# Kernel tuning notes

Measured on AMD Instinct MI355X. Metric: run time of the kernel, lower is better.

Reference implementation:

```python
import jax, jax.numpy as jnp
import numpy as np

E, D, I, TOPK, N = 8, 2048, 4096, 2, 4096


def setup_inputs() -> dict:
    key = jax.random.key(0)
    k_x, k_w, k_i, k_g, k_u, k_d = jax.random.split(key, 6)
    x = jax.random.normal(k_x, (N, D), dtype=jnp.float32)
    expert_weights = jax.random.uniform(k_w, (N, TOPK), dtype=jnp.float32)
    expert_indices = jax.random.randint(k_i, (N, TOPK), 0, E).astype(jnp.int32)
    s_in = np.float32(1.0 / np.sqrt(D))
    s_mid = np.float32(1.0 / np.sqrt(I))
    # SwitchLinear weights: [num_experts, out_features, in_features]
    wg = jax.random.normal(k_g, (E, I, D), dtype=jnp.float32) * s_in
    wu = jax.random.normal(k_u, (E, I, D), dtype=jnp.float32) * s_in
    wd = jax.random.normal(k_d, (E, D, I), dtype=jnp.float32) * s_mid
    return {"x": x, "expert_weights": expert_weights,
            "expert_indices": expert_indices, "top_k": TOPK,
            "wg": wg, "wu": wu, "wd": wd}


def reference(x, expert_weights, expert_indices, top_k, wg, wu, wd):
    # out[n] = sum_k expert_weights[n,k] * Wd[e] @ (silu(Wg[e] x[n]) * (Wu[e] x[n]))
    #          with e = expert_indices[n,k].
    # Grouped-by-expert form (identical math): accumulate each expert's
    # contribution over all tokens, weighted by its routing weight (0 if not routed).
    num_experts = wg.shape[0]
    out = jnp.zeros_like(x)
    for e in range(num_experts):
        # per-token routing weight for expert e (sums over top_k slots)
        w_e = jnp.sum(jnp.where(expert_indices == e, expert_weights, 0.0), axis=-1)  # [N]
        gate = x @ wg[e].T            # [N, I]
        up = x @ wu[e].T              # [N, I]
        h = jax.nn.silu(gate) * up    # SwiGLU, [N, I]
        out = out + w_e[:, None] * (h @ wd[e].T)  # [N, D]
    return out
```

## Files before the change

### kernel.cpp

```cpp
#include <hip/hip_runtime.h>
#include <hip/hip_bf16.h>
#include <math.h>

#define E_ 8
#define D_ 2048
#define I_ 4096
#define TOPK_ 2
#define N_ 4096
#define NPAIR (N_*TOPK_)
#define PADMAX 10240
#define MAXTB256 40
#define MAXTB128 72

typedef __attribute__((ext_vector_type(8))) short s8v;
typedef __attribute__((ext_vector_type(8))) unsigned short us8;
typedef __attribute__((ext_vector_type(4))) float f32x4;
typedef const __attribute__((address_space(1))) void* gvp;
typedef __attribute__((address_space(3))) void* lvp;

__device__ __forceinline__ unsigned short f2bf(float f) {
  union { float f; unsigned int u; } c; c.f = f;
  unsigned int u = c.u;
  u += 0x7fffu + ((u >> 16) & 1u);
  return (unsigned short)(u >> 16);
}

__global__ void route_kernel(const int* __restrict__ idx, const float* __restrict__ ew,
                             int pad,
                             int* cnt, int* offs, int* tb, int* ntb,
                             int* perm, float* wgt)
{
  __shared__ int scnt[E_], soff[E_ + 1], scur[E_];
  int t = threadIdx.x;
  if (t < E_) scnt[t] = 0;
  __syncthreads();
  for (int p = t; p < NPAIR; p += blockDim.x) atomicAdd(&scnt[idx[p]], 1);
  __syncthreads();
  if (t == 0) {
    int o = 0;
    for (int e = 0; e < E_; e++) {
      soff[e] = o; scur[e] = o;
      o += ((scnt[e] + pad - 1) / pad) * pad;
    }
    soff[E_] = o;
    int T = 0;
    for (int e = 0; e < E_; e++) {
      int nb = (scnt[e] + pad - 1) / pad;
      for (int rb = 0; rb < nb; rb++) tb[T++] = (e << 16) | rb;
    }
    *ntb = T;
    for (int e = 0; e < E_; e++) { cnt[e] = scnt[e]; offs[e] = soff[e]; }
    offs[E_] = o;
  }
  __syncthreads();
  for (int e = 0; e < E_; e++) {
    int start = soff[e] + scnt[e], end = soff[e + 1];
    for (int s = start + t; s < end; s += blockDim.x) { perm[s] = -1; wgt[s] = 0.f; }
  }
  __syncthreads();
  for (int p = t; p < NPAIR; p += blockDim.x) {
    int e = idx[p];
    int pos = atomicAdd(&scur[e], 1);
    perm[pos] = p / TOPK_;
    wgt[pos]  = ew[p];
  }
}

__global__ __launch_bounds__(256)
void cvt8_kernel(const float* __restrict__ src, unsigned short* __restrict__ dst)
{
  size_t i = ((size_t)blockIdx.x * 256 + threadIdx.x) * 8;
  float4 a = *(const float4*)(src + i);
  float4 b = *(const float4*)(src + i + 4);
  us8 o;
  o[0]=f2bf(a.x); o[1]=f2bf(a.y); o[2]=f2bf(a.z); o[3]=f2bf(a.w);
  o[4]=f2bf(b.x); o[5]=f2bf(b.y); o[6]=f2bf(b.z); o[7]=f2bf(b.w);
  *(us8*)(dst + i) = o;
}

__global__ __launch_bounds__(256)
void cvtw_kernel(const float* __restrict__ s0, const float* __restrict__ s1,
                 const float* __restrict__ s2,
                 unsigned short* __restrict__ d0, unsigned short* __restrict__ d1,
                 unsigned short* __restrict__ d2)
{
  int b = blockIdx.x;
  int which = b >> 15, bi = b & 32767;
  const float* s = which == 0 ? s0 : (which == 1 ? s1 : s2);
  unsigned short* d = which == 0 ? d0 : (which == 1 ? d1 : d2);
  size_t i = ((size_t)bi * 256 + threadIdx.x) * 8;
  float4 a = *(const float4*)(s + i);
  float4 bb = *(const float4*)(s + i + 4);
  us8 o;
  o[0]=f2bf(a.x); o[1]=f2bf(a.y); o[2]=f2bf(a.z); o[3]=f2bf(a.w);
  o[4]=f2bf(bb.x); o[5]=f2bf(bb.y); o[6]=f2bf(bb.z); o[7]=f2bf(bb.w);
  *(us8*)(d + i) = o;
}

#define A_SLAB(P,KH) (((P)*2+(KH))*8192)
#define B_SLAB(P,KH) (32768 + ((P)*2+(KH))*8192)

#define SB  __builtin_amdgcn_sched_barrier(0)
#define BARR __builtin_amdgcn_s_barrier()
#define VMW(N) asm volatile("s_waitcnt vmcnt(" #N ")" ::: "memory")
#define LGK asm volatile("s_waitcnt lgkmcnt(0)" ::: "memory")

#define LOAD_A(P,KH,MH) { \
  const unsigned short* ap_ = &smem[A_SLAB(P,KH) + aBase + (MH)*2048]; \
  af[0] = *(const s8v*)(ap_);      af[1] = *(const s8v*)(ap_+512); \
  af[2] = *(const s8v*)(ap_+1024); af[3] = *(const s8v*)(ap_+1536); }

#define LOAD_B(P,KH) { \
  const unsigned short* bp_ = &smem[B_SLAB(P,KH) + bBase]; \
  bf[0] = *(const s8v*)(bp_);      bf[1] = *(const s8v*)(bp_+512); \
  bf[2] = *(const s8v*)(bp_+1024); bf[3] = *(const s8v*)(bp_+1536); }

#define STAGE_A(T,KH,P) { \
  __builtin_amdgcn_global_load_lds((gvp)(aptr0 + (T)*64 + (KH)*32), (lvp)(&smem[A_SLAB(P,KH) + (w*2+0)*512]), 16, 0, 0); \
  __builtin_amdgcn_global_load_lds((gvp)(aptr1 + (T)*64 + (KH)*32), (lvp)(&smem[A_SLAB(P,KH) + (w*2+1)*512]), 16, 0, 0); }

#define STAGE_B(T,KH,P) { \
  __builtin_amdgcn_global_load_lds((gvp)(bptr0 + (T)*64 + (KH)*32), (lvp)(&smem[B_SLAB(P,KH) + (w*2+0)*512]), 16, 0, 0); \
  __builtin_amdgcn_global_load_lds((gvp)(bptr1 + (T)*64 + (KH)*32), (lvp)(&smem[B_SLAB(P,KH) + (w*2+1)*512]), 16, 0, 0); }

#define MFMA16(MH) { \
  _Pragma("unroll") for (int m_ = 0; m_ < 4; m_++) \
    _Pragma("unroll") for (int n_ = 0; n_ < 4; n_++) \
      acc[(MH)*4+m_][n_] = __builtin_amdgcn_mfma_f32_16x16x32_bf16(af[m_], bf[n_], acc[(MH)*4+m_][n_], 0, 0, 0); }

#define TILE_PHASES(T, P, Pn, NT_) { \
  if (T) { VMW(4); SB; } \
  LOAD_B(P, 0); LOAD_A(P, 0, 0); \
  if ((T) + 1 < (NT_)) { STAGE_A((T)+1, 1, Pn); } \
  SB; BARR; LGK; SB; \
  __builtin_amdgcn_s_setprio(1); MFMA16(0); __builtin_amdgcn_s_setprio(0); \
  SB; BARR; SB; \
  LOAD_A(P, 0, 1); \
  if ((T) + 1 < (NT_)) { STAGE_B((T)+1, 1, Pn); } \
  SB; BARR; LGK; SB; \
  __builtin_amdgcn_s_setprio(1); MFMA16(1); __builtin_amdgcn_s_setprio(0); \
  SB; BARR; SB; \
  if ((T) == (NT_) - 1) { VMW(0); SB; } else { VMW(4); SB; } \
  LOAD_B(P, 1); LOAD_A(P, 1, 0); \
  if ((T) + 2 < (NT_)) { STAGE_A((T)+2, 0, P); } \
  SB; BARR; LGK; SB; \
  __builtin_amdgcn_s_setprio(1); MFMA16(0); __builtin_amdgcn_s_setprio(0); \
  SB; BARR; SB; \
  LOAD_A(P, 1, 1); \
  if ((T) + 2 < (NT_)) { STAGE_B((T)+2, 0, P); } \
  SB; BARR; LGK; SB; \
  __builtin_amdgcn_s_setprio(1); MFMA16(1); __builtin_amdgcn_s_setprio(0); \
  SB; BARR; SB; }

#define K_LOOP(NT_) { \
  STAGE_A(0,0,0); STAGE_B(0,0,0); STAGE_A(0,1,0); STAGE_B(0,1,0); \
  STAGE_A(1,0,1); STAGE_B(1,0,1); \
  VMW(8); SB; BARR; SB; \
  _Pragma("unroll 1") \
  for (int tt = 0; tt < (NT_)/2; ++tt) { \
    int t0_ = 2*tt, t1_ = 2*tt+1; \
    TILE_PHASES(t0_, 0, 1, NT_); \
    TILE_PHASES(t1_, 1, 0, NT_); \
  } }

__global__ __launch_bounds__(512, 2)
void gu8_kernel(const unsigned short* __restrict__ xb,
                const unsigned short* __restrict__ wgb,
                const unsigned short* __restrict__ wub,
                const int* __restrict__ tb, const int* __restrict__ ntb,
                const int* __restrict__ offs, const int* __restrict__ perm,
                unsigned short* __restrict__ H)
{
  __shared__ unsigned short smem[65536];

  int nwg = gridDim.x * gridDim.y;
  int lid = blockIdx.y * gridDim.x + blockIdx.x;
  int cpx = nwg >> 3;
  int sid = (lid & 7) * cpx + (lid >> 3);
  int bx = sid % gridDim.x;
  int by = sid / gridDim.x;
  if (bx >= *ntb) return;
  int ent = tb[bx];
  int e = ent >> 16, rb = ent & 0xffff;
  int slotbase = offs[e] + rb * 256;
  int i0 = by * 128;

  int tid = threadIdx.x, lane = tid & 63, w = tid >> 6;
  int wr = w >> 2, wc = w & 3;

  int cS = (lane & 7) ^ (lane >> 3);
  int rrS = 2 * (lane >> 3) + (cS >> 2);
  int kcS = (cS & 3) * 8;
  int ar0 = (w * 2 + 0) * 16 + rrS;
  int tk0 = perm[slotbase + ar0];       if (tk0 < 0) tk0 = 0;
  int tk1 = perm[slotbase + ar0 + 16];  if (tk1 < 0) tk1 = 0;
  const unsigned short* aptr0 = xb + (size_t)tk0 * D_ + kcS;
  const unsigned short* aptr1 = xb + (size_t)tk1 * D_ + kcS;
  const unsigned short* bptr0 = wgb + ((size_t)e * I_ + i0 + w * 16 + rrS) * D_ + kcS;
  const unsigned short* bptr1 = wub + ((size_t)e * I_ + i0 + w * 16 + rrS) * D_ + kcS;

  int hl = (lane & 15) >> 1;
  int pA = (((lane & 1) * 4 + (lane >> 4)) ^ hl) * 8;
  int aBase = wr * 4096 + hl * 64 + pA;
  int bBase = wc * 2048 + hl * 64 + pA;

  s8v af[4], bf[4];
  f32x4 acc[8][4];
#pragma unroll
  for (int m = 0; m < 8; m++)
#pragma unroll
    for (int n = 0; n < 4; n++) acc[m][n] = f32x4{0.f,0.f,0.f,0.f};

  K_LOOP(32);

#pragma unroll
  for (int m = 0; m < 8; m++) {
#pragma unroll
    for (int r = 0; r < 4; r++) {
      int row = wr * 128 + m * 16 + (lane >> 4) * 4 + r;
      size_t hbase = (size_t)(slotbase + row) * I_ + i0 + (lane & 15);
#pragma unroll
      for (int pr = 0; pr < 2; pr++) {
        float g = acc[m][pr*2][r];
        float u = acc[m][pr*2+1][r];
        float h = (g / (1.0f + __expf(-g))) * u;
        H[hbase + (wc * 2 + pr) * 16] = f2bf(h);
      }
    }
  }
}

__global__ __launch_bounds__(512, 2)
void down8_kernel(const unsigned short* __restrict__ H,
                  const unsigned short* __restrict__ wdb,
                  const int* __restrict__ tb, const int* __restrict__ ntb,
                  const int* __restrict__ offs, const int* __restrict__ perm,
                  const float* __restrict__ wgt,
                  float* __restrict__ out)
{
  __shared__ unsigned short smem[65536];

  int nwg = gridDim.x * gridDim.y;
  int lid = blockIdx.y * gridDim.x + blockIdx.x;
  int cpx = nwg >> 3;
  int sid = (lid & 7) * cpx + (lid >> 3);
  int bx = sid % gridDim.x;
  int by = sid / gridDim.x;
  if (bx >= *ntb) return;
  int ent = tb[bx];
  int e = ent >> 16, rb = ent & 0xffff;
  int slotbase = offs[e] + rb * 256;
  int d0 = by * 256;

  int tid = threadIdx.x, lane = tid & 63, w = tid >> 6;
  int wr = w >> 2, wc = w & 3;

  int cS = (lane & 7) ^ (lane >> 3);
  int rrS = 2 * (lane >> 3) + (cS >> 2);
  int kcS = (cS & 3) * 8;
  int ar0 = (w * 2 + 0) * 16 + rrS;
  const unsigned short* aptr0 = H + (size_t)(slotbase + ar0) * I_ + kcS;
  const unsigned short* aptr1 = H + (size_t)(slotbase + ar0 + 16) * I_ + kcS;
  const unsigned short* bptr0 = wdb + ((size_t)e * D_ + d0 + (w*2+0)*16 + rrS) * I_ + kcS;
  const unsigned short* bptr1 = wdb + ((size_t)e * D_ + d0 + (w*2+1)*16 + rrS) * I_ + kcS;

  int hl = (lane & 15) >> 1;
  int pA = (((lane & 1) * 4 + (lane >> 4)) ^ hl) * 8;
  int aBase = wr * 4096 + hl * 64 + pA;
  int bBase = wc * 2048 + hl * 64 + pA;

  s8v af[4], bf[4];
  f32x4 acc[8][4];
#pragma unroll
  for (int m = 0; m < 8; m++)
#pragma unroll
    for (int n = 0; n < 4; n++) acc[m][n] = f32x4{0.f,0.f,0.f,0.f};

  K_LOOP(64);

#pragma unroll
  for (int m = 0; m < 8; m++) {
#pragma unroll
    for (int r = 0; r < 4; r++) {
      int row = wr * 128 + m * 16 + (lane >> 4) * 4 + r;
      int s = slotbase + row;
      int tok = perm[s];
      if (tok < 0) continue;
      float wv = wgt[s];
      float* op = out + (size_t)tok * D_ + d0 + wc * 64 + (lane & 15);
#pragma unroll
      for (int n = 0; n < 4; n++)
        atomicAdd(op + n * 16, acc[m][n][r] * wv);
    }
  }
}

__device__ __forceinline__ void cvt16(const float* __restrict__ src, unsigned short* dst) {
  float4 a = *(const float4*)(src);
  float4 b = *(const float4*)(src + 4);
  float4 c = *(const float4*)(src + 8);
  float4 d = *(const float4*)(src + 12);
  us8 o0, o1;
  o0[0]=f2bf(a.x); o0[1]=f2bf(a.y); o0[2]=f2bf(a.z); o0[3]=f2bf(a.w);
  o0[4]=f2bf(b.x); o0[5]=f2bf(b.y); o0[6]=f2bf(b.z); o0[7]=f2bf(b.w);
  o1[0]=f2bf(c.x); o1[1]=f2bf(c.y); o1[2]=f2bf(c.z); o1[3]=f2bf(c.w);
  o1[4]=f2bf(d.x); o1[5]=f2bf(d.y); o1[6]=f2bf(d.z); o1[7]=f2bf(d.w);
  *(us8*)(dst)     = o0;
  *(us8*)(dst + 8) = o1;
}

__global__ __launch_bounds__(256)
void gu_f32_kernel(const unsigned short* __restrict__ xb,
                   const float* __restrict__ wg, const float* __restrict__ wu,
                   const int* __restrict__ tb, const int* __restrict__ ntb,
                   const int* __restrict__ offs, const int* __restrict__ perm,
                   unsigned short* __restrict__ H)
{
  int bx = blockIdx.x;
  if (bx >= *ntb) return;
  int ent = tb[bx];
  int e = ent >> 16, rb = ent & 0xffff;
  int slotbase = offs[e] + rb * 128;
  int i0 = blockIdx.y * 64;

  __shared__ unsigned short Al[128 * 64];
  __shared__ unsigned short Bgl[64 * 64];
  __shared__ unsigned short Bul[64 * 64];

  int tid = threadIdx.x;
  int lane = tid & 63, w = tid >> 6;
  int wr = w >> 1, wc = w & 1;

  const unsigned short* asrc[4];
#pragma unroll
  for (int q = 0; q < 4; q++) {
    int r = (w * 4 + q) * 8 + (lane >> 3);
    int tok = perm[slotbase + r];
    if (tok < 0) tok = 0;
    asrc[q] = xb + (size_t)tok * D_ + (lane & 7) * 8;
  }
  int brow = tid >> 2;
  int bk = (tid & 3) * 16;
  const float* gsrc = wg + ((size_t)e * I_ + i0 + brow) * D_ + bk;
  const float* usrc = wu + ((size_t)e * I_ + i0 + brow) * D_ + bk;

  f32x4 accg[4][2], accu[4][2];
#pragma unroll
  for (int m = 0; m < 4; m++)
#pragma unroll
    for (int n = 0; n < 2; n++) {
      accg[m][n] = f32x4{0.f, 0.f, 0.f, 0.f};
      accu[m][n] = f32x4{0.f, 0.f, 0.f, 0.f};
    }

  for (int k0 = 0; k0 < D_; k0 += 64) {
#pragma unroll
    for (int q = 0; q < 4; q++)
      __builtin_amdgcn_global_load_lds((gvp)(asrc[q] + k0), (lvp)(&Al[(w * 4 + q) * 512]), 16, 0, 0);
    cvt16(gsrc + k0, &Bgl[brow * 64 + bk]);
    cvt16(usrc + k0, &Bul[brow * 64 + bk]);
    __syncthreads();
#pragma unroll
    for (int kk = 0; kk < 2; kk++) {
      int kb = kk * 32 + (lane >> 4) * 8;
      s8v af[4], bg[2], bu[2];
#pragma unroll
      for (int m = 0; m < 4; m++)
        af[m] = *(const s8v*)(&Al[(wr * 64 + m * 16 + (lane & 15)) * 64 + kb]);
#pragma unroll
      for (int n = 0; n < 2; n++) {
        int col = wc * 32 + n * 16 + (lane & 15);
        bg[n] = *(const s8v*)(&Bgl[col * 64 + kb]);
        bu[n] = *(const s8v*)(&Bul[col * 64 + kb]);
      }
#pragma unroll
      for (int m = 0; m < 4; m++)
#pragma unroll
        for (int n = 0; n < 2; n++) {
          accg[m][n] = __builtin_amdgcn_mfma_f32_16x16x32_bf16(af[m], bg[n], accg[m][n], 0, 0, 0);
          accu[m][n] = __builtin_amdgcn_mfma_f32_16x16x32_bf16(af[m], bu[n], accu[m][n], 0, 0, 0);
        }
    }
    __syncthreads();
  }

  int colbase = i0 + wc * 32;
#pragma unroll
  for (int m = 0; m < 4; m++) {
#pragma unroll
    for (int r = 0; r < 4; r++) {
      int row = wr * 64 + m * 16 + (lane >> 4) * 4 + r;
      size_t s = (size_t)(slotbase + row) * I_;
#pragma unroll
      for (int n = 0; n < 2; n++) {
        float g = accg[m][n][r];
        float u = accu[m][n][r];
        float h = (g / (1.0f + __expf(-g))) * u;
        H[s + colbase + n * 16 + (lane & 15)] = f2bf(h);
      }
    }
  }
}

__global__ __launch_bounds__(256)
void down_f32_kernel(const unsigned short* __restrict__ H,
                     const float* __restrict__ wd,
                     const int* __restrict__ tb, const int* __restrict__ ntb,
                     const int* __restrict__ offs, const int* __restrict__ perm,
                     const float* __restrict__ wgt,
                     float* __restrict__ out)
{
  int bx = blockIdx.x;
  if (bx >= *ntb) return;
  int ent = tb[bx];
  int e = ent >> 16, rb = ent & 0xffff;
  int slotbase = offs[e] + rb * 128;
  int d0 = blockIdx.y * 128;

  __shared__ unsigned short Al[128 * 64];
  __shared__ unsigned short Bl[128 * 64];

  int tid = threadIdx.x, lane = tid & 63, w = tid >> 6;
  int wr = w >> 1, wc = w & 1;

  const unsigned short* asrc[4];
#pragma unroll
  for (int q = 0; q < 4; q++) {
    int r = (w * 4 + q) * 8 + (lane >> 3);
    asrc[q] = H + (size_t)(slotbase + r) * I_ + (lane & 7) * 8;
  }
  int brow = tid >> 1;
  int bk = (tid & 1) * 32;
  const float* bsrc = wd + ((size_t)e * D_ + d0 + brow) * I_ + bk;

  f32x4 acc[4][4];
#pragma unroll
  for (int m = 0; m < 4; m++)
#pragma unroll
    for (int n = 0; n < 4; n++) acc[m][n] = f32x4{0.f, 0.f, 0.f, 0.f};

  for (int k0 = 0; k0 < I_; k0 += 64) {
#pragma unroll
    for (int q = 0; q < 4; q++)
      __builtin_amdgcn_global_load_lds((gvp)(asrc[q] + k0), (lvp)(&Al[(w * 4 + q) * 512]), 16, 0, 0);
    cvt16(bsrc + k0,      &Bl[brow * 64 + bk]);
    cvt16(bsrc + k0 + 16, &Bl[brow * 64 + bk + 16]);
    __syncthreads();
#pragma unroll
    for (int kk = 0; kk < 2; kk++) {
      int kb = kk * 32 + (lane >> 4) * 8;
      s8v af[4], bfr[4];
#pragma unroll
      for (int m = 0; m < 4; m++)
        af[m] = *(const s8v*)(&Al[(wr * 64 + m * 16 + (lane & 15)) * 64 + kb]);
#pragma unroll
      for (int n = 0; n < 4; n++)
        bfr[n] = *(const s8v*)(&Bl[(wc * 64 + n * 16 + (lane & 15)) * 64 + kb]);
#pragma unroll
      for (int m = 0; m < 4; m++)
#pragma unroll
        for (int n = 0; n < 4; n++)
          acc[m][n] = __builtin_amdgcn_mfma_f32_16x16x32_bf16(af[m], bfr[n], acc[m][n], 0, 0, 0);
    }
    __syncthreads();
  }

#pragma unroll
  for (int m = 0; m < 4; m++) {
#pragma unroll
    for (int r = 0; r < 4; r++) {
      int row = wr * 64 + m * 16 + (lane >> 4) * 4 + r;
      int s = slotbase + row;
      int tok = perm[s];
      if (tok < 0) continue;
      float wv = wgt[s];
      float* op = out + (size_t)tok * D_ + d0 + wc * 64;
#pragma unroll
      for (int n = 0; n < 4; n++)
        atomicAdd(op + n * 16 + (lane & 15), acc[m][n][r] * wv);
    }
  }
}

extern "C" void kernel_launch(void* const* d_in, const int* in_sizes, int n_in,
                              void* d_out, int out_size, void* d_ws, size_t ws_size,
                              hipStream_t stream)
{
  const float* x  = (const float*)d_in[0];
  const float* ew = (const float*)d_in[1];
  const int*  idx = (const int*)d_in[2];
  const float* wg = (const float*)d_in[4];
  const float* wu = (const float*)d_in[5];
  const float* wd = (const float*)d_in[6];
  float* out = (float*)d_out;

  char* ws = (char*)d_ws;
  int* cnt   = (int*)(ws);
  int* ntb   = (int*)(ws + 64);
  int* tb    = (int*)(ws + 128);
  int* offs  = (int*)(ws + 640);
  int* perm  = (int*)(ws + 4096);
  float* wgt = (float*)(ws + 4096 + PADMAX * 4);

  const size_t xb_off  = 131072;
  const size_t xb_b    = (size_t)N_ * D_ * 2;
  const size_t H_b     = (size_t)PADMAX * I_ * 2;
  const size_t w_b     = (size_t)E_ * I_ * D_ * 2;
  unsigned short* xb  = (unsigned short*)(ws + xb_off);
  unsigned short* H   = (unsigned short*)(ws + xb_off + xb_b);
  unsigned short* wgb = (unsigned short*)(ws + xb_off + xb_b + H_b);
  unsigned short* wub = (unsigned short*)((char*)wgb + w_b);
  unsigned short* wdb = (unsigned short*)((char*)wub + w_b);
  size_t need = xb_off + xb_b + H_b + 3 * w_b;

  hipMemsetAsync(d_out, 0, (size_t)N_ * D_ * sizeof(float), stream);
  cvt8_kernel<<<(N_ * D_ / 8) / 256, 256, 0, stream>>>(x, xb);

  if (ws_size >= need) {
    route_kernel<<<1, 256, 0, stream>>>(idx, ew, 256, cnt, offs, tb, ntb, perm, wgt);
    cvtw_kernel<<<3 * 32768, 256, 0, stream>>>(wg, wu, wd, wgb, wub, wdb);
    gu8_kernel<<<dim3(MAXTB256, I_ / 128), 512, 0, stream>>>(xb, wgb, wub, tb, ntb, offs, perm, H);
    down8_kernel<<<dim3(MAXTB256, D_ / 256), 512, 0, stream>>>(H, wdb, tb, ntb, offs, perm, wgt, out);
  } else {
    route_kernel<<<1, 256, 0, stream>>>(idx, ew, 128, cnt, offs, tb, ntb, perm, wgt);
    gu_f32_kernel<<<dim3(MAXTB128, I_ / 64), 256, 0, stream>>>(xb, wg, wu, tb, ntb, offs, perm, H);
    down_f32_kernel<<<dim3(MAXTB128, D_ / 128), 256, 0, stream>>>(H, wd, tb, ntb, offs, perm, wgt, out);
  }
}
```

Baseline: 832.2 us.

## Fuse fp32-to-bf16 weight conversion into GEMM B-tile staging, drop cvtw pass

Removes the separate pass that converted all three expert weight tensors to bf16 in workspace. The gate/up and down GEMM kernels now load fp32 weights into registers, convert them to bf16 in-kernel and write them to LDS, using a reworked software pipeline with register staging and adjusted waitcnts. This avoids writing and rereading a bf16 weight copy each call. In exchange each GEMM reads twice the weight bytes per tile, adds VALU conversion work and register pressure, and each weight tile is reloaded and reconverted by every token-block workgroup that uses it.

```diff
diff --git a/kernel.cpp b/kernel.cpp
--- a/kernel.cpp
+++ b/kernel.cpp
@@ -10,7 +10,6 @@
 #define NPAIR (N_*TOPK_)
 #define PADMAX 10240
 #define MAXTB256 40
-#define MAXTB128 72
 
 typedef __attribute__((ext_vector_type(8))) short s8v;
 typedef __attribute__((ext_vector_type(8))) unsigned short us8;
@@ -78,25 +77,6 @@
   *(us8*)(dst + i) = o;
 }
 
-__global__ __launch_bounds__(256)
-void cvtw_kernel(const float* __restrict__ s0, const float* __restrict__ s1,
-                 const float* __restrict__ s2,
-                 unsigned short* __restrict__ d0, unsigned short* __restrict__ d1,
-                 unsigned short* __restrict__ d2)
-{
-  int b = blockIdx.x;
-  int which = b >> 15, bi = b & 32767;
-  const float* s = which == 0 ? s0 : (which == 1 ? s1 : s2);
-  unsigned short* d = which == 0 ? d0 : (which == 1 ? d1 : d2);
-  size_t i = ((size_t)bi * 256 + threadIdx.x) * 8;
-  float4 a = *(const float4*)(s + i);
-  float4 bb = *(const float4*)(s + i + 4);
-  us8 o;
-  o[0]=f2bf(a.x); o[1]=f2bf(a.y); o[2]=f2bf(a.z); o[3]=f2bf(a.w);
-  o[4]=f2bf(bb.x); o[5]=f2bf(bb.y); o[6]=f2bf(bb.z); o[7]=f2bf(bb.w);
-  *(us8*)(d + i) = o;
-}
-
 #define A_SLAB(P,KH) (((P)*2+(KH))*8192)
 #define B_SLAB(P,KH) (32768 + ((P)*2+(KH))*8192)
 
@@ -104,6 +84,8 @@
 #define BARR __builtin_amdgcn_s_barrier()
 #define VMW(N) asm volatile("s_waitcnt vmcnt(" #N ")" ::: "memory")
 #define LGK asm volatile("s_waitcnt lgkmcnt(0)" ::: "memory")
+#define PRIO1 __builtin_amdgcn_s_setprio(1)
+#define PRIO0 __builtin_amdgcn_s_setprio(0)
 
 #define LOAD_A(P,KH,MH) { \
   const unsigned short* ap_ = &smem[A_SLAB(P,KH) + aBase + (MH)*2048]; \
@@ -119,9 +101,19 @@
   __builtin_amdgcn_global_load_lds((gvp)(aptr0 + (T)*64 + (KH)*32), (lvp)(&smem[A_SLAB(P,KH) + (w*2+0)*512]), 16, 0, 0); \
   __builtin_amdgcn_global_load_lds((gvp)(aptr1 + (T)*64 + (KH)*32), (lvp)(&smem[A_SLAB(P,KH) + (w*2+1)*512]), 16, 0, 0); }
 
-#define STAGE_B(T,KH,P) { \
-  __builtin_amdgcn_global_load_lds((gvp)(bptr0 + (T)*64 + (KH)*32), (lvp)(&smem[B_SLAB(P,KH) + (w*2+0)*512]), 16, 0, 0); \
-  __builtin_amdgcn_global_load_lds((gvp)(bptr1 + (T)*64 + (KH)*32), (lvp)(&smem[B_SLAB(P,KH) + (w*2+1)*512]), 16, 0, 0); }
+#define ISSUE_B(T,KH,Q) { \
+  int o_ = (T)*64 + (KH)*32; \
+  xq[Q][0] = *(const float4*)(bsrc0 + o_); xq[Q][1] = *(const float4*)(bsrc0 + o_ + 4); \
+  xq[Q][2] = *(const float4*)(bsrc1 + o_); xq[Q][3] = *(const float4*)(bsrc1 + o_ + 4); }
+
+#define CVT_WRITE(Q,P,KH) { \
+  us8 o0_, o1_; \
+  o0_[0]=f2bf(xq[Q][0].x); o0_[1]=f2bf(xq[Q][0].y); o0_[2]=f2bf(xq[Q][0].z); o0_[3]=f2bf(xq[Q][0].w); \
+  o0_[4]=f2bf(xq[Q][1].x); o0_[5]=f2bf(xq[Q][1].y); o0_[6]=f2bf(xq[Q][1].z); o0_[7]=f2bf(xq[Q][1].w); \
+  o1_[0]=f2bf(xq[Q][2].x); o1_[1]=f2bf(xq[Q][2].y); o1_[2]=f2bf(xq[Q][2].z); o1_[3]=f2bf(xq[Q][2].w); \
+  o1_[4]=f2bf(xq[Q][3].x); o1_[5]=f2bf(xq[Q][3].y); o1_[6]=f2bf(xq[Q][3].z); o1_[7]=f2bf(xq[Q][3].w); \
+  *(us8*)(&smem[B_SLAB(P,KH) + (w*2+0)*512 + lane*8]) = o0_; \
+  *(us8*)(&smem[B_SLAB(P,KH) + (w*2+1)*512 + lane*8]) = o1_; }
 
 #define MFMA16(MH) { \
   _Pragma("unroll") for (int m_ = 0; m_ < 4; m_++) \
@@ -129,44 +121,51 @@
       acc[(MH)*4+m_][n_] = __builtin_amdgcn_mfma_f32_16x16x32_bf16(af[m_], bf[n_], acc[(MH)*4+m_][n_], 0, 0, 0); }
 
 #define TILE_PHASES(T, P, Pn, NT_) { \
-  if (T) { VMW(4); SB; } \
-  LOAD_B(P, 0); LOAD_A(P, 0, 0); \
-  if ((T) + 1 < (NT_)) { STAGE_A((T)+1, 1, Pn); } \
+  int tn1_ = (T)+1 < (NT_) ? (T)+1 : (NT_)-1; \
+  int tn2_ = (T)+2 < (NT_) ? (T)+2 : (NT_)-1; \
+   \
+  LOAD_B(P,0); LOAD_A(P,0,0); \
+  STAGE_A(tn1_, 1, Pn); \
   SB; BARR; LGK; SB; \
-  __builtin_amdgcn_s_setprio(1); MFMA16(0); __builtin_amdgcn_s_setprio(0); \
-  SB; BARR; SB; \
-  LOAD_A(P, 0, 1); \
-  if ((T) + 1 < (NT_)) { STAGE_B((T)+1, 1, Pn); } \
+  PRIO1; MFMA16(0); PRIO0; SB; BARR; SB; \
+   \
+  LOAD_A(P,0,1); \
+  ISSUE_B(tn1_, 1, 1); \
+  VMW(6); SB; \
+  CVT_WRITE(0, Pn, 0); \
   SB; BARR; LGK; SB; \
-  __builtin_amdgcn_s_setprio(1); MFMA16(1); __builtin_amdgcn_s_setprio(0); \
-  SB; BARR; SB; \
-  if ((T) == (NT_) - 1) { VMW(0); SB; } else { VMW(4); SB; } \
-  LOAD_B(P, 1); LOAD_A(P, 1, 0); \
-  if ((T) + 2 < (NT_)) { STAGE_A((T)+2, 0, P); } \
+  PRIO1; MFMA16(1); PRIO0; SB; BARR; SB; \
+   \
+  LOAD_B(P,1); LOAD_A(P,1,0); \
+  STAGE_A(tn2_, 0, P); \
   SB; BARR; LGK; SB; \
-  __builtin_amdgcn_s_setprio(1); MFMA16(0); __builtin_amdgcn_s_setprio(0); \
-  SB; BARR; SB; \
-  LOAD_A(P, 1, 1); \
-  if ((T) + 2 < (NT_)) { STAGE_B((T)+2, 0, P); } \
+  PRIO1; MFMA16(0); PRIO0; SB; BARR; SB; \
+   \
+  LOAD_A(P,1,1); \
+  ISSUE_B(tn2_, 0, 0); \
+  VMW(6); SB; \
+  CVT_WRITE(1, Pn, 1); \
   SB; BARR; LGK; SB; \
-  __builtin_amdgcn_s_setprio(1); MFMA16(1); __builtin_amdgcn_s_setprio(0); \
-  SB; BARR; SB; }
+  PRIO1; MFMA16(1); PRIO0; SB; BARR; SB; }
 
 #define K_LOOP(NT_) { \
-  STAGE_A(0,0,0); STAGE_B(0,0,0); STAGE_A(0,1,0); STAGE_B(0,1,0); \
-  STAGE_A(1,0,1); STAGE_B(1,0,1); \
-  VMW(8); SB; BARR; SB; \
+  STAGE_A(0,0,0); STAGE_A(0,1,0); \
+  ISSUE_B(0,0,0); ISSUE_B(0,1,1); \
+  VMW(0); SB; \
+  CVT_WRITE(0,0,0); CVT_WRITE(1,0,1); \
+  STAGE_A(1,0,1); \
+  ISSUE_B(1,0,0); \
+  LGK; SB; BARR; SB; \
   _Pragma("unroll 1") \
   for (int tt = 0; tt < (NT_)/2; ++tt) { \
-    int t0_ = 2*tt, t1_ = 2*tt+1; \
-    TILE_PHASES(t0_, 0, 1, NT_); \
-    TILE_PHASES(t1_, 1, 0, NT_); \
+    TILE_PHASES(2*tt,   0, 1, NT_); \
+    TILE_PHASES(2*tt+1, 1, 0, NT_); \
   } }
 
 __global__ __launch_bounds__(512, 2)
 void gu8_kernel(const unsigned short* __restrict__ xb,
-                const unsigned short* __restrict__ wgb,
-                const unsigned short* __restrict__ wub,
+                const float* __restrict__ wg,
+                const float* __restrict__ wu,
                 const int* __restrict__ tb, const int* __restrict__ ntb,
                 const int* __restrict__ offs, const int* __restrict__ perm,
                 unsigned short* __restrict__ H)
@@ -196,8 +195,8 @@
   int tk1 = perm[slotbase + ar0 + 16];  if (tk1 < 0) tk1 = 0;
   const unsigned short* aptr0 = xb + (size_t)tk0 * D_ + kcS;
   const unsigned short* aptr1 = xb + (size_t)tk1 * D_ + kcS;
-  const unsigned short* bptr0 = wgb + ((size_t)e * I_ + i0 + w * 16 + rrS) * D_ + kcS;
-  const unsigned short* bptr1 = wub + ((size_t)e * I_ + i0 + w * 16 + rrS) * D_ + kcS;
+  const float* bsrc0 = wg + ((size_t)e * I_ + i0 + w * 16 + rrS) * D_ + kcS;
+  const float* bsrc1 = wu + ((size_t)e * I_ + i0 + w * 16 + rrS) * D_ + kcS;
 
   int hl = (lane & 15) >> 1;
   int pA = (((lane & 1) * 4 + (lane >> 4)) ^ hl) * 8;
@@ -205,6 +204,7 @@
   int bBase = wc * 2048 + hl * 64 + pA;
 
   s8v af[4], bf[4];
+  float4 xq[2][4];
   f32x4 acc[8][4];
 #pragma unroll
   for (int m = 0; m < 8; m++)
@@ -232,7 +232,7 @@
 
 __global__ __launch_bounds__(512, 2)
 void down8_kernel(const unsigned short* __restrict__ H,
-                  const unsigned short* __restrict__ wdb,
+                  const float* __restrict__ wd,
                   const int* __restrict__ tb, const int* __restrict__ ntb,
                   const int* __restrict__ offs, const int* __restrict__ perm,
                   const float* __restrict__ wgt,
@@ -261,8 +261,8 @@
   int ar0 = (w * 2 + 0) * 16 + rrS;
   const unsigned short* aptr0 = H + (size_t)(slotbase + ar0) * I_ + kcS;
   const unsigned short* aptr1 = H + (size_t)(slotbase + ar0 + 16) * I_ + kcS;
-  const unsigned short* bptr0 = wdb + ((size_t)e * D_ + d0 + (w*2+0)*16 + rrS) * I_ + kcS;
-  const unsigned short* bptr1 = wdb + ((size_t)e * D_ + d0 + (w*2+1)*16 + rrS) * I_ + kcS;
+  const float* bsrc0 = wd + ((size_t)e * D_ + d0 + (w*2+0)*16 + rrS) * I_ + kcS;
+  const float* bsrc1 = wd + ((size_t)e * D_ + d0 + (w*2+1)*16 + rrS) * I_ + kcS;
 
   int hl = (lane & 15) >> 1;
   int pA = (((lane & 1) * 4 + (lane >> 4)) ^ hl) * 8;
@@ -270,6 +270,7 @@
   int bBase = wc * 2048 + hl * 64 + pA;
 
   s8v af[4], bf[4];
+  float4 xq[2][4];
   f32x4 acc[8][4];
 #pragma unroll
   for (int m = 0; m < 8; m++)
@@ -295,193 +296,6 @@
   }
 }
 
-__device__ __forceinline__ void cvt16(const float* __restrict__ src, unsigned short* dst) {
-  float4 a = *(const float4*)(src);
-  float4 b = *(const float4*)(src + 4);
-  float4 c = *(const float4*)(src + 8);
-  float4 d = *(const float4*)(src + 12);
-  us8 o0, o1;
-  o0[0]=f2bf(a.x); o0[1]=f2bf(a.y); o0[2]=f2bf(a.z); o0[3]=f2bf(a.w);
-  o0[4]=f2bf(b.x); o0[5]=f2bf(b.y); o0[6]=f2bf(b.z); o0[7]=f2bf(b.w);
-  o1[0]=f2bf(c.x); o1[1]=f2bf(c.y); o1[2]=f2bf(c.z); o1[3]=f2bf(c.w);
-  o1[4]=f2bf(d.x); o1[5]=f2bf(d.y); o1[6]=f2bf(d.z); o1[7]=f2bf(d.w);
-  *(us8*)(dst)     = o0;
-  *(us8*)(dst + 8) = o1;
-}
-
-__global__ __launch_bounds__(256)
-void gu_f32_kernel(const unsigned short* __restrict__ xb,
-                   const float* __restrict__ wg, const float* __restrict__ wu,
-                   const int* __restrict__ tb, const int* __restrict__ ntb,
-                   const int* __restrict__ offs, const int* __restrict__ perm,
-                   unsigned short* __restrict__ H)
-{
-  int bx = blockIdx.x;
-  if (bx >= *ntb) return;
-  int ent = tb[bx];
-  int e = ent >> 16, rb = ent & 0xffff;
-  int slotbase = offs[e] + rb * 128;
-  int i0 = blockIdx.y * 64;
-
-  __shared__ unsigned short Al[128 * 64];
-  __shared__ unsigned short Bgl[64 * 64];
-  __shared__ unsigned short Bul[64 * 64];
-
-  int tid = threadIdx.x;
-  int lane = tid & 63, w = tid >> 6;
-  int wr = w >> 1, wc = w & 1;
-
-  const unsigned short* asrc[4];
-#pragma unroll
-  for (int q = 0; q < 4; q++) {
-    int r = (w * 4 + q) * 8 + (lane >> 3);
-    int tok = perm[slotbase + r];
-    if (tok < 0) tok = 0;
-    asrc[q] = xb + (size_t)tok * D_ + (lane & 7) * 8;
-  }
-  int brow = tid >> 2;
-  int bk = (tid & 3) * 16;
-  const float* gsrc = wg + ((size_t)e * I_ + i0 + brow) * D_ + bk;
-  const float* usrc = wu + ((size_t)e * I_ + i0 + brow) * D_ + bk;
-
-  f32x4 accg[4][2], accu[4][2];
-#pragma unroll
-  for (int m = 0; m < 4; m++)
-#pragma unroll
-    for (int n = 0; n < 2; n++) {
-      accg[m][n] = f32x4{0.f, 0.f, 0.f, 0.f};
-      accu[m][n] = f32x4{0.f, 0.f, 0.f, 0.f};
-    }
-
-  for (int k0 = 0; k0 < D_; k0 += 64) {
-#pragma unroll
-    for (int q = 0; q < 4; q++)
-      __builtin_amdgcn_global_load_lds((gvp)(asrc[q] + k0), (lvp)(&Al[(w * 4 + q) * 512]), 16, 0, 0);
-    cvt16(gsrc + k0, &Bgl[brow * 64 + bk]);
-    cvt16(usrc + k0, &Bul[brow * 64 + bk]);
-    __syncthreads();
-#pragma unroll
-    for (int kk = 0; kk < 2; kk++) {
-      int kb = kk * 32 + (lane >> 4) * 8;
-      s8v af[4], bg[2], bu[2];
-#pragma unroll
-      for (int m = 0; m < 4; m++)
-        af[m] = *(const s8v*)(&Al[(wr * 64 + m * 16 + (lane & 15)) * 64 + kb]);
-#pragma unroll
-      for (int n = 0; n < 2; n++) {
-        int col = wc * 32 + n * 16 + (lane & 15);
-        bg[n] = *(const s8v*)(&Bgl[col * 64 + kb]);
-        bu[n] = *(const s8v*)(&Bul[col * 64 + kb]);
-      }
-#pragma unroll
-      for (int m = 0; m < 4; m++)
-#pragma unroll
-        for (int n = 0; n < 2; n++) {
-          accg[m][n] = __builtin_amdgcn_mfma_f32_16x16x32_bf16(af[m], bg[n], accg[m][n], 0, 0, 0);
-          accu[m][n] = __builtin_amdgcn_mfma_f32_16x16x32_bf16(af[m], bu[n], accu[m][n], 0, 0, 0);
-        }
-    }
-    __syncthreads();
-  }
-
-  int colbase = i0 + wc * 32;
-#pragma unroll
-  for (int m = 0; m < 4; m++) {
-#pragma unroll
-    for (int r = 0; r < 4; r++) {
-      int row = wr * 64 + m * 16 + (lane >> 4) * 4 + r;
-      size_t s = (size_t)(slotbase + row) * I_;
-#pragma unroll
-      for (int n = 0; n < 2; n++) {
-        float g = accg[m][n][r];
-        float u = accu[m][n][r];
-        float h = (g / (1.0f + __expf(-g))) * u;
-        H[s + colbase + n * 16 + (lane & 15)] = f2bf(h);
-      }
-    }
-  }
-}
-
-__global__ __launch_bounds__(256)
-void down_f32_kernel(const unsigned short* __restrict__ H,
-                     const float* __restrict__ wd,
-                     const int* __restrict__ tb, const int* __restrict__ ntb,
-                     const int* __restrict__ offs, const int* __restrict__ perm,
-                     const float* __restrict__ wgt,
-                     float* __restrict__ out)
-{
-  int bx = blockIdx.x;
-  if (bx >= *ntb) return;
-  int ent = tb[bx];
-  int e = ent >> 16, rb = ent & 0xffff;
-  int slotbase = offs[e] + rb * 128;
-  int d0 = blockIdx.y * 128;
-
-  __shared__ unsigned short Al[128 * 64];
-  __shared__ unsigned short Bl[128 * 64];
-
-  int tid = threadIdx.x, lane = tid & 63, w = tid >> 6;
-  int wr = w >> 1, wc = w & 1;
-
-  const unsigned short* asrc[4];
-#pragma unroll
-  for (int q = 0; q < 4; q++) {
-    int r = (w * 4 + q) * 8 + (lane >> 3);
-    asrc[q] = H + (size_t)(slotbase + r) * I_ + (lane & 7) * 8;
-  }
-  int brow = tid >> 1;
-  int bk = (tid & 1) * 32;
-  const float* bsrc = wd + ((size_t)e * D_ + d0 + brow) * I_ + bk;
-
-  f32x4 acc[4][4];
-#pragma unroll
-  for (int m = 0; m < 4; m++)
-#pragma unroll
-    for (int n = 0; n < 4; n++) acc[m][n] = f32x4{0.f, 0.f, 0.f, 0.f};
-
-  for (int k0 = 0; k0 < I_; k0 += 64) {
-#pragma unroll
-    for (int q = 0; q < 4; q++)
-      __builtin_amdgcn_global_load_lds((gvp)(asrc[q] + k0), (lvp)(&Al[(w * 4 + q) * 512]), 16, 0, 0);
-    cvt16(bsrc + k0,      &Bl[brow * 64 + bk]);
-    cvt16(bsrc + k0 + 16, &Bl[brow * 64 + bk + 16]);
-    __syncthreads();
-#pragma unroll
-    for (int kk = 0; kk < 2; kk++) {
-      int kb = kk * 32 + (lane >> 4) * 8;
-      s8v af[4], bfr[4];
-#pragma unroll
-      for (int m = 0; m < 4; m++)
-        af[m] = *(const s8v*)(&Al[(wr * 64 + m * 16 + (lane & 15)) * 64 + kb]);
-#pragma unroll
-      for (int n = 0; n < 4; n++)
-        bfr[n] = *(const s8v*)(&Bl[(wc * 64 + n * 16 + (lane & 15)) * 64 + kb]);
-#pragma unroll
-      for (int m = 0; m < 4; m++)
-#pragma unroll
-        for (int n = 0; n < 4; n++)
-          acc[m][n] = __builtin_amdgcn_mfma_f32_16x16x32_bf16(af[m], bfr[n], acc[m][n], 0, 0, 0);
-    }
-    __syncthreads();
-  }
-
-#pragma unroll
-  for (int m = 0; m < 4; m++) {
-#pragma unroll
-    for (int r = 0; r < 4; r++) {
-      int row = wr * 64 + m * 16 + (lane >> 4) * 4 + r;
-      int s = slotbase + row;
-      int tok = perm[s];
-      if (tok < 0) continue;
-      float wv = wgt[s];
-      float* op = out + (size_t)tok * D_ + d0 + wc * 64;
-#pragma unroll
-      for (int n = 0; n < 4; n++)
-        atomicAdd(op + n * 16 + (lane & 15), acc[m][n][r] * wv);
-    }
-  }
-}
-
 extern "C" void kernel_launch(void* const* d_in, const int* in_sizes, int n_in,
                               void* d_out, int out_size, void* d_ws, size_t ws_size,
                               hipStream_t stream)
@@ -502,28 +316,14 @@
   int* perm  = (int*)(ws + 4096);
   float* wgt = (float*)(ws + 4096 + PADMAX * 4);
 
-  const size_t xb_off  = 131072;
-  const size_t xb_b    = (size_t)N_ * D_ * 2;
-  const size_t H_b     = (size_t)PADMAX * I_ * 2;
-  const size_t w_b     = (size_t)E_ * I_ * D_ * 2;
-  unsigned short* xb  = (unsigned short*)(ws + xb_off);
-  unsigned short* H   = (unsigned short*)(ws + xb_off + xb_b);
-  unsigned short* wgb = (unsigned short*)(ws + xb_off + xb_b + H_b);
-  unsigned short* wub = (unsigned short*)((char*)wgb + w_b);
-  unsigned short* wdb = (unsigned short*)((char*)wub + w_b);
-  size_t need = xb_off + xb_b + H_b + 3 * w_b;
+  const size_t xb_off = 131072;
+  const size_t xb_b   = (size_t)N_ * D_ * 2;
+  unsigned short* xb = (unsigned short*)(ws + xb_off);
+  unsigned short* H  = (unsigned short*)(ws + xb_off + xb_b);
 
   hipMemsetAsync(d_out, 0, (size_t)N_ * D_ * sizeof(float), stream);
+  route_kernel<<<1, 256, 0, stream>>>(idx, ew, 256, cnt, offs, tb, ntb, perm, wgt);
   cvt8_kernel<<<(N_ * D_ / 8) / 256, 256, 0, stream>>>(x, xb);
-
-  if (ws_size >= need) {
-    route_kernel<<<1, 256, 0, stream>>>(idx, ew, 256, cnt, offs, tb, ntb, perm, wgt);
-    cvtw_kernel<<<3 * 32768, 256, 0, stream>>>(wg, wu, wd, wgb, wub, wdb);
-    gu8_kernel<<<dim3(MAXTB256, I_ / 128), 512, 0, stream>>>(xb, wgb, wub, tb, ntb, offs, perm, H);
-    down8_kernel<<<dim3(MAXTB256, D_ / 256), 512, 0, stream>>>(H, wdb, tb, ntb, offs, perm, wgt, out);
-  } else {
-    route_kernel<<<1, 256, 0, stream>>>(idx, ew, 128, cnt, offs, tb, ntb, perm, wgt);
-    gu_f32_kernel<<<dim3(MAXTB128, I_ / 64), 256, 0, stream>>>(xb, wg, wu, tb, ntb, offs, perm, H);
-    down_f32_kernel<<<dim3(MAXTB128, D_ / 128), 256, 0, stream>>>(H, wd, tb, ntb, offs, perm, wgt, out);
-  }
-}
+  gu8_kernel<<<dim3(MAXTB256, I_ / 128), 512, 0, stream>>>(xb, wg, wu, tb, ntb, offs, perm, H);
+  down8_kernel<<<dim3(MAXTB256, D_ / 256), 512, 0, stream>>>(H, wd, tb, ntb, offs, perm, wgt, out);
+}
```

Result: slower. 1.027 ms (+23.4%).
